# Kernel optimization log

Hardware: AMD Instinct MI355X
Metric: run time of the kernel (lower is better)

Reference implementation:

```python
import jax, jax.numpy as jnp
import numpy as np

N_NODES = 50000
N_EDGES = 819200  # divisible by num_rels=8 -> equal relation segments (implicit rel_ptr)
NUM_RELS = 8
N_HEADS = 4
IN_FEAT = 256
OUT_FEAT = 128
HEAD_DIM = OUT_FEAT // N_HEADS
LEAKY_SLOPE = 0.2


def setup_inputs() -> dict:
    key = jax.random.key(0)
    ks = jax.random.split(key, 7)
    inputs = jax.random.normal(ks[0], (N_NODES, IN_FEAT), dtype=jnp.float32)
    conv_weights = jax.random.normal(ks[1], (NUM_RELS, N_HEADS, IN_FEAT, HEAD_DIM), dtype=jnp.float32) * (1.0 / np.sqrt(IN_FEAT))
    attn_l = jax.random.normal(ks[2], (NUM_RELS, N_HEADS, HEAD_DIM), dtype=jnp.float32) * 0.1
    attn_r = jax.random.normal(ks[3], (NUM_RELS, N_HEADS, HEAD_DIM), dtype=jnp.float32) * 0.1
    h_bias = jax.random.normal(ks[4], (OUT_FEAT,), dtype=jnp.float32) * 0.01
    row_idx = jax.random.randint(ks[5], (N_EDGES,), 0, N_NODES, dtype=jnp.int32)
    col_idx = jax.random.randint(ks[6], (N_EDGES,), 0, N_NODES, dtype=jnp.int32)
    return {
        'inputs': inputs,
        'conv_weights': conv_weights,
        'attn_l': attn_l,
        'attn_r': attn_r,
        'h_bias': h_bias,
        'row_idx': row_idx,
        'col_idx': col_idx,
    }


def reference(inputs, conv_weights, attn_l, attn_r, h_bias, row_idx, col_idx):
    R, H, IN, D = conv_weights.shape
    E = row_idx.shape[0]
    N = inputs.shape[0]
    epr = E // R  # edges per relation (equal segments == rel_ptr)

    # relation-grouped GEMM: per-edge transformed src features [R, epr, H, D]
    src = inputs[row_idx].reshape(R, epr, IN)
    feat_src = jnp.einsum('rei,rhid->rehd', src, conv_weights)
    el = jnp.einsum('rehd,rhd->reh', feat_src, attn_l)

    dst = inputs[col_idx].reshape(R, epr, IN)
    feat_dst = jnp.einsum('rei,rhid->rehd', dst, conv_weights)
    er = jnp.einsum('rehd,rhd->reh', feat_dst, attn_r)

    # fused GAT: leaky_relu(el+er), softmax over incoming edges per dst node
    e = jax.nn.leaky_relu((el + er).reshape(E, H), negative_slope=LEAKY_SLOPE)
    m = jax.ops.segment_max(e, col_idx, num_segments=N)          # [N, H]
    e_exp = jnp.exp(e - m[col_idx])                              # [E, H]
    denom = jax.ops.segment_sum(e_exp, col_idx, num_segments=N)  # [N, H]
    alpha = e_exp / denom[col_idx]                               # [E, H]

    feat = feat_src.reshape(E, H, D)
    h = jax.ops.segment_sum(alpha[:, :, None] * feat, col_idx, num_segments=N)  # [N, H, D]
    h = h.reshape(N, H * D) + h_bias
    # activation=None, self_loop=False, dropout treated as eval (identity)
    return h
```

## Files before the change

### kernel.cpp

```cpp
#include <hip/hip_runtime.h>
#include <hip/hip_bf16.h>

#define N_NODES 50000
#define N_EDGES 819200
#define NUM_RELS 8
#define EPR (N_EDGES / NUM_RELS)
#define N_HEADS 4
#define IN_FEAT 256
#define OUT_FEAT 128
#define HEAD_DIM 32
#define NB_SCAN ((N_NODES + 255) / 256)

typedef __attribute__((ext_vector_type(8))) __bf16 bf16x8;
typedef __attribute__((ext_vector_type(4))) __bf16 bf16x4;
typedef __attribute__((ext_vector_type(4))) float f32x4;

#define SZ_FEAT ((size_t)NUM_RELS * N_NODES * OUT_FEAT)
#define SZ_EL ((size_t)NUM_RELS * N_NODES * N_HEADS)
#define SZ_WB ((size_t)IN_FEAT * 64)
#define SZ_WT ((size_t)NUM_RELS * OUT_FEAT * IN_FEAT / 2)
#define OFF_FEAT ((size_t)0)
#define OFF_XB (OFF_FEAT + SZ_FEAT / 2)
#define OFF_EL (OFF_FEAT + SZ_FEAT)
#define OFF_ER (OFF_EL + SZ_EL)
#define OFF_WB (OFF_ER + SZ_EL)
#define OFF_WT (OFF_WB + SZ_WB)
#define OFF_INT (OFF_WT + SZ_WT)
#define IOFF_CNT ((size_t)0)
#define IOFF_PTR ((size_t)N_NODES)
#define IOFF_CUR ((size_t)2 * N_NODES)
#define IOFF_BSUM ((size_t)3 * N_NODES)
#define IOFF_SPAY ((size_t)3 * N_NODES + 256)

__device__ __forceinline__ void gload16(const void* g, void* l) {
    __builtin_amdgcn_global_load_lds(
        (const __attribute__((address_space(1))) unsigned int*)g,
        (__attribute__((address_space(3))) unsigned int*)l, 16, 0, 0);
}

__global__ void k_cvtx(const float* __restrict__ x, __bf16* __restrict__ xb) {
    int tid = blockIdx.x * blockDim.x + threadIdx.x;
    if (tid >= N_NODES * 32) return;
    int n = tid >> 5, sg = tid & 31;
    const float* xp = x + (size_t)n * IN_FEAT + sg * 8;
    float4 a = *(const float4*)xp;
    float4 b = *(const float4*)(xp + 4);
    bf16x8 v;
    v[0] = (__bf16)a.x; v[1] = (__bf16)a.y; v[2] = (__bf16)a.z; v[3] = (__bf16)a.w;
    v[4] = (__bf16)b.x; v[5] = (__bf16)b.y; v[6] = (__bf16)b.z; v[7] = (__bf16)b.w;
    int slot = (sg & ~7) | ((sg & 7) ^ (n & 7));
    *(bf16x8*)(xb + (size_t)n * 256 + slot * 8) = v;
}

__global__ void k_cvtw(const float* __restrict__ cw, __bf16* __restrict__ wtl) {
    int tid = blockIdx.x * blockDim.x + threadIdx.x;
    if (tid >= 32768) return;
    int s = tid & 3, brow = (tid >> 2) & 127, ks = (tid >> 9) & 1, kc = (tid >> 10) & 3, r = tid >> 12;
    int q = s ^ ((brow >> 1) & 3);
    int k0 = kc * 64 + ks * 32 + q * 8;
    int h = brow >> 5, d = brow & 31;
    const float* src = cw + ((size_t)(r * N_HEADS + h) * IN_FEAT + k0) * HEAD_DIM + d;
    bf16x8 v;
#pragma unroll
    for (int j = 0; j < 8; ++j) v[j] = (__bf16)src[j * HEAD_DIM];
    *(bf16x8*)(wtl + (size_t)tid * 8) = v;
}

__global__ void k_wboth(const float* __restrict__ cw, const float* __restrict__ al,
                        const float* __restrict__ ar, __bf16* __restrict__ wbt) {
    int tid = blockIdx.x * blockDim.x + threadIdx.x;
    if (tid >= IN_FEAT * 64) return;
    int col = tid >> 8, i = tid & 255;
    int side = col >> 5, r = (col >> 2) & 7, h = col & 3;
    const float* av = (side ? ar : al) + (size_t)(r * N_HEADS + h) * HEAD_DIM;
    const float* cwp = cw + ((size_t)(r * N_HEADS + h) * IN_FEAT + i) * HEAD_DIM;
    float s = 0.f;
#pragma unroll
    for (int d = 0; d < HEAD_DIM; ++d) s += cwp[d] * av[d];
    wbt[(size_t)col * IN_FEAT + i] = (__bf16)s;
}

__global__ void k_wbimg(const __bf16* __restrict__ wbt, __bf16* __restrict__ wbl) {
    int tid = blockIdx.x * blockDim.x + threadIdx.x;
    if (tid >= 2048) return;
    int s = tid & 3, brow = (tid >> 2) & 63, ks = (tid >> 8) & 1, kc = tid >> 9;
    int q = s ^ ((brow >> 1) & 3);
    int k0 = kc * 64 + ks * 32 + q * 8;
    bf16x8 v = *(const bf16x8*)(wbt + (size_t)brow * IN_FEAT + k0);
    *(bf16x8*)(wbl + (size_t)tid * 8) = v;
}

__global__ __launch_bounds__(256, 2) void k_fused(const __bf16* __restrict__ xb,
                                                  const __bf16* __restrict__ wtl,
                                                  const __bf16* __restrict__ wbl,
                                                  __bf16* __restrict__ featb,
                                                  float* __restrict__ el,
                                                  float* __restrict__ er) {
    __shared__ __align__(16) unsigned char sA[65536];
    __shared__ __align__(16) unsigned char sB[16384];
    const int t = threadIdx.x, lane = t & 63, w = t >> 6;
    const int wr = w >> 1, wc = w & 1;
    const int n0 = blockIdx.x * 128;

#pragma unroll
    for (int i = 0; i < 16; ++i) {
        int off = i * 4096 + w * 1024 + lane * 16;
        int row = off >> 9;
        int n = n0 + row;
        if (n >= N_NODES) n = N_NODES - 1;
        gload16((const char*)xb + (size_t)n * 512 + (off & 511), sA + i * 4096 + w * 1024);
    }
#pragma unroll
    for (int i = 0; i < 2; ++i)
        gload16((const char*)wtl + i * 4096 + w * 1024 + lane * 16, sB + i * 4096 + w * 1024);

    f32x4 acc[4][4];
#pragma unroll
    for (int i = 0; i < 4; ++i)
#pragma unroll
        for (int j = 0; j < 4; ++j) acc[i][j] = (f32x4){0.f, 0.f, 0.f, 0.f};

    for (int item = 0; item < 64; ++item) {
        const int buf = item & 1;
        if (item < 63) {
            const char* ch = (const char*)wtl + (size_t)(item + 1) * 8192;
#pragma unroll
            for (int i = 0; i < 2; ++i)
                gload16(ch + i * 4096 + w * 1024 + lane * 16, sB + (buf ^ 1) * 8192 + i * 4096 + w * 1024);
            asm volatile("s_waitcnt vmcnt(2)" ::: "memory");
        } else {
            gload16((const char*)wbl + w * 1024 + lane * 16, sB + (buf ^ 1) * 8192 + w * 1024);
            asm volatile("s_waitcnt vmcnt(1)" ::: "memory");
        }
        __builtin_amdgcn_s_barrier();
        __builtin_amdgcn_sched_barrier(0);

        const int r = item >> 3, kc = (item >> 1) & 3, ks = item & 1;
        bf16x8 af[4], bg[4];
#pragma unroll
        for (int rb = 0; rb < 4; ++rb) {
            int row = wr * 64 + rb * 16 + (lane & 15);
            int slot = kc * 8 + ((ks * 4 + (lane >> 4)) ^ (row & 7));
            af[rb] = *(const bf16x8*)(sA + row * 512 + slot * 16);
        }
#pragma unroll
        for (int cb = 0; cb < 4; ++cb) {
            int brow = wc * 64 + cb * 16 + (lane & 15);
            int s = (lane >> 4) ^ ((brow >> 1) & 3);
            bg[cb] = *(const bf16x8*)(sB + buf * 8192 + brow * 64 + s * 16);
        }
#pragma unroll
        for (int rb = 0; rb < 4; ++rb)
#pragma unroll
            for (int cb = 0; cb < 4; ++cb)
                acc[rb][cb] = __builtin_amdgcn_mfma_f32_16x16x32_bf16(af[rb], bg[cb], acc[rb][cb], 0, 0, 0);

        if ((item & 7) == 7) {
#pragma unroll
            for (int rb = 0; rb < 4; ++rb)
#pragma unroll
                for (int q = 0; q < 4; ++q) {
                    int rowi = wr * 64 + rb * 16 + (lane >> 4) * 4 + q;
                    int n = n0 + rowi;
                    if (n < N_NODES) {
                        __bf16* fp = featb + ((size_t)r * N_NODES + n) * OUT_FEAT + wc * 64 + (lane & 15);
#pragma unroll
                        for (int cb = 0; cb < 4; ++cb) fp[cb * 16] = (__bf16)acc[rb][cb][q];
                    }
                }
#pragma unroll
            for (int i = 0; i < 4; ++i)
#pragma unroll
                for (int j = 0; j < 4; ++j) acc[i][j] = (f32x4){0.f, 0.f, 0.f, 0.f};
        }
        asm volatile("" ::: "memory");
        __builtin_amdgcn_s_barrier();
    }

    f32x4 acc2[4][2];
#pragma unroll
    for (int i = 0; i < 4; ++i)
#pragma unroll
        for (int j = 0; j < 2; ++j) acc2[i][j] = (f32x4){0.f, 0.f, 0.f, 0.f};

    for (int e = 0; e < 8; ++e) {
        const int buf = e & 1;
        if (e < 7) {
            gload16((const char*)wbl + (size_t)(e + 1) * 4096 + w * 1024 + lane * 16,
                    sB + (buf ^ 1) * 8192 + w * 1024);
            asm volatile("s_waitcnt vmcnt(1)" ::: "memory");
        } else {
            asm volatile("s_waitcnt vmcnt(0)" ::: "memory");
        }
        __builtin_amdgcn_s_barrier();
        __builtin_amdgcn_sched_barrier(0);

        const int kc = e >> 1, ks = e & 1;
        bf16x8 af[4], bg[2];
#pragma unroll
        for (int rb = 0; rb < 4; ++rb) {
            int row = wr * 64 + rb * 16 + (lane & 15);
            int slot = kc * 8 + ((ks * 4 + (lane >> 4)) ^ (row & 7));
            af[rb] = *(const bf16x8*)(sA + row * 512 + slot * 16);
        }
#pragma unroll
        for (int cb = 0; cb < 2; ++cb) {
            int brow = wc * 32 + cb * 16 + (lane & 15);
            int s = (lane >> 4) ^ ((brow >> 1) & 3);
            bg[cb] = *(const bf16x8*)(sB + buf * 8192 + brow * 64 + s * 16);
        }
#pragma unroll
        for (int rb = 0; rb < 4; ++rb)
#pragma unroll
            for (int cb = 0; cb < 2; ++cb)
                acc2[rb][cb] = __builtin_amdgcn_mfma_f32_16x16x32_bf16(af[rb], bg[cb], acc2[rb][cb], 0, 0, 0);
        asm volatile("" ::: "memory");
        __builtin_amdgcn_s_barrier();
    }
#pragma unroll
    for (int rb = 0; rb < 4; ++rb)
#pragma unroll
        for (int q = 0; q < 4; ++q) {
            int n = n0 + wr * 64 + rb * 16 + (lane >> 4) * 4 + q;
            if (n < N_NODES) {
#pragma unroll
                for (int cb = 0; cb < 2; ++cb) {
                    int c = wc * 32 + cb * 16 + (lane & 15);
                    int side = c >> 5, rr = (c >> 2) & 7, h = c & 3;
                    float* dst = side ? er : el;
                    dst[((size_t)rr * N_NODES + n) * N_HEADS + h] = acc2[rb][cb][q];
                }
            }
        }
}

__global__ void k_hist(const int* __restrict__ col, int* __restrict__ cnt) {
    int e = blockIdx.x * blockDim.x + threadIdx.x;
    if (e < N_EDGES) atomicAdd(cnt + col[e], 1);
}

__global__ __launch_bounds__(256) void k_scanA(const int* __restrict__ cnt,
                                               int* __restrict__ excl,
                                               int* __restrict__ bsum) {
    __shared__ int s[256];
    int i = blockIdx.x * 256 + threadIdx.x;
    int v = (i < N_NODES) ? cnt[i] : 0;
    s[threadIdx.x] = v;
    __syncthreads();
#pragma unroll
    for (int off = 1; off < 256; off <<= 1) {
        int t = (threadIdx.x >= off) ? s[threadIdx.x - off] : 0;
        __syncthreads();
        s[threadIdx.x] += t;
        __syncthreads();
    }
    if (i < N_NODES) excl[i] = s[threadIdx.x] - v;
    if (threadIdx.x == 255) bsum[blockIdx.x] = s[255];
}

__global__ __launch_bounds__(256) void k_scanB(int* __restrict__ bsum) {
    __shared__ int s[256];
    int v = (threadIdx.x < NB_SCAN) ? bsum[threadIdx.x] : 0;
    s[threadIdx.x] = v;
    __syncthreads();
#pragma unroll
    for (int off = 1; off < 256; off <<= 1) {
        int t = (threadIdx.x >= off) ? s[threadIdx.x - off] : 0;
        __syncthreads();
        s[threadIdx.x] += t;
        __syncthreads();
    }
    bsum[threadIdx.x] = s[threadIdx.x] - v;
}

__global__ __launch_bounds__(256) void k_scanC(int* __restrict__ ptr,
                                               int* __restrict__ cursor,
                                               const int* __restrict__ bsum) {
    int i = blockIdx.x * 256 + threadIdx.x;
    if (i >= N_NODES) return;
    int p = ptr[i] + bsum[blockIdx.x];
    ptr[i] = p;
    cursor[i] = p;
}

__global__ void k_scatter(const int* __restrict__ row, const int* __restrict__ col,
                          int* __restrict__ cursor, int* __restrict__ spay) {
    int e = blockIdx.x * blockDim.x + threadIdx.x;
    if (e >= N_EDGES) return;
    int c = col[e];
    int pos = atomicAdd(cursor + c, 1);
    spay[pos] = row[e] | ((e / EPR) << 20);
}

__global__ __launch_bounds__(256) void k_agg(const int* __restrict__ ptr,
                                             const int* __restrict__ cnt,
                                             const int* __restrict__ spay,
                                             const float* __restrict__ el,
                                             const float* __restrict__ er,
                                             const __bf16* __restrict__ featb,
                                             const float* __restrict__ bias,
                                             float* __restrict__ out) {
    const int wv = threadIdx.x >> 6, lane = threadIdx.x & 63;
    const int n = blockIdx.x * 4 + wv;
    if (n >= N_NODES) return;
    const int start = ptr[n], len = cnt[n];
    const int h = lane >> 4;
    float accx = 0.f, accy = 0.f, den = 0.f;
    int j = 0;
    for (; j + 4 <= len; j += 4) {
        int p[4];
#pragma unroll
        for (int u = 0; u < 4; ++u) p[u] = spay[start + j + u];
        float w[4], vx[4], vy[4];
#pragma unroll
        for (int u = 0; u < 4; ++u) {
            int rw = p[u] & 0xFFFFF, r = p[u] >> 20;
            size_t rb = (size_t)r * N_NODES;
            float s = el[(rb + rw) * N_HEADS + h] + er[(rb + n) * N_HEADS + h];
            s = s > 0.f ? s : 0.2f * s;
            w[u] = __expf(s);
            ushort2 raw = *(const ushort2*)(featb + (rb + rw) * OUT_FEAT + lane * 2);
            vx[u] = __uint_as_float((unsigned)raw.x << 16);
            vy[u] = __uint_as_float((unsigned)raw.y << 16);
        }
#pragma unroll
        for (int u = 0; u < 4; ++u) {
            accx += w[u] * vx[u];
            accy += w[u] * vy[u];
            den += w[u];
        }
    }
    for (; j < len; ++j) {
        int p = spay[start + j];
        int rw = p & 0xFFFFF, r = p >> 20;
        size_t rb = (size_t)r * N_NODES;
        float s = el[(rb + rw) * N_HEADS + h] + er[(rb + n) * N_HEADS + h];
        s = s > 0.f ? s : 0.2f * s;
        float w = __expf(s);
        ushort2 raw = *(const ushort2*)(featb + (rb + rw) * OUT_FEAT + lane * 2);
        accx += w * __uint_as_float((unsigned)raw.x << 16);
        accy += w * __uint_as_float((unsigned)raw.y << 16);
        den += w;
    }
    float inv = (len > 0) ? 1.f / den : 0.f;
    int o = lane * 2;
    float2 res;
    res.x = accx * inv + bias[o];
    res.y = accy * inv + bias[o + 1];
    *(float2*)(out + (size_t)n * OUT_FEAT + o) = res;
}

extern "C" void kernel_launch(void* const* d_in, const int* in_sizes, int n_in,
                              void* d_out, int out_size, void* d_ws, size_t ws_size,
                              hipStream_t stream) {
    const float* x = (const float*)d_in[0];
    const float* cw = (const float*)d_in[1];
    const float* al = (const float*)d_in[2];
    const float* ar = (const float*)d_in[3];
    const float* bias = (const float*)d_in[4];
    const int* row = (const int*)d_in[5];
    const int* col = (const int*)d_in[6];
    float* out = (float*)d_out;
    float* ws = (float*)d_ws;

    __bf16* featb = (__bf16*)(ws + OFF_FEAT);
    __bf16* xb = (__bf16*)(ws + OFF_XB);
    float* el = ws + OFF_EL;
    float* er = ws + OFF_ER;
    __bf16* wbt = (__bf16*)(ws + OFF_WB);
    __bf16* wbl = (__bf16*)(ws + OFF_WB + 8192);
    __bf16* wtl = (__bf16*)(ws + OFF_WT);
    int* iw = (int*)(ws + OFF_INT);
    int* cnt = iw + IOFF_CNT;
    int* ptr = iw + IOFF_PTR;
    int* cur = iw + IOFF_CUR;
    int* bsum = iw + IOFF_BSUM;
    int* spay = iw + IOFF_SPAY;

    hipMemsetAsync(cnt, 0, N_NODES * sizeof(int), stream);

    k_cvtx<<<(N_NODES * 32 + 255) / 256, 256, 0, stream>>>(x, xb);
    k_cvtw<<<128, 256, 0, stream>>>(cw, wtl);
    k_wboth<<<(IN_FEAT * 64 + 255) / 256, 256, 0, stream>>>(cw, al, ar, wbt);
    k_wbimg<<<8, 256, 0, stream>>>(wbt, wbl);
    k_fused<<<(N_NODES + 127) / 128, 256, 0, stream>>>(xb, wtl, wbl, featb, el, er);

    k_hist<<<(N_EDGES + 255) / 256, 256, 0, stream>>>(col, cnt);
    k_scanA<<<NB_SCAN, 256, 0, stream>>>(cnt, ptr, bsum);
    k_scanB<<<1, 256, 0, stream>>>(bsum);
    k_scanC<<<NB_SCAN, 256, 0, stream>>>(ptr, cur, bsum);
    k_scatter<<<(N_EDGES + 255) / 256, 256, 0, stream>>>(row, col, cur, spay);

    k_agg<<<(N_NODES + 3) / 4, 256, 0, stream>>>(ptr, cnt, spay, el, er, featb, bias, out);
}
```

Measured before the change: 234.1 us.

## Fuse fp32-to-bf16 input conversion into GEMM kernel and halve node tile

Removes the standalone k_cvtx pass and instead loads fp32 node features directly in k_fused, converting them to bf16 and writing them into the swizzled LDS layout. This avoids writing and re-reading a bf16 copy of the input plus one kernel launch. The node tile shrinks from 128 to 64 rows, so shared memory per block drops and launch bounds now target 3 blocks per CU. The trade-offs are that weight tiles are re-streamed by twice as many blocks and the A-load becomes a synchronous register path instead of async global-to-LDS loads.

```diff
diff --git a/kernel.cpp b/kernel.cpp
--- a/kernel.cpp
+++ b/kernel.cpp
@@ -20,7 +20,6 @@
 #define SZ_WB ((size_t)IN_FEAT * 64)
 #define SZ_WT ((size_t)NUM_RELS * OUT_FEAT * IN_FEAT / 2)
 #define OFF_FEAT ((size_t)0)
-#define OFF_XB (OFF_FEAT + SZ_FEAT / 2)
 #define OFF_EL (OFF_FEAT + SZ_FEAT)
 #define OFF_ER (OFF_EL + SZ_EL)
 #define OFF_WB (OFF_ER + SZ_EL)
@@ -38,20 +37,6 @@
         (__attribute__((address_space(3))) unsigned int*)l, 16, 0, 0);
 }
 
-__global__ void k_cvtx(const float* __restrict__ x, __bf16* __restrict__ xb) {
-    int tid = blockIdx.x * blockDim.x + threadIdx.x;
-    if (tid >= N_NODES * 32) return;
-    int n = tid >> 5, sg = tid & 31;
-    const float* xp = x + (size_t)n * IN_FEAT + sg * 8;
-    float4 a = *(const float4*)xp;
-    float4 b = *(const float4*)(xp + 4);
-    bf16x8 v;
-    v[0] = (__bf16)a.x; v[1] = (__bf16)a.y; v[2] = (__bf16)a.z; v[3] = (__bf16)a.w;
-    v[4] = (__bf16)b.x; v[5] = (__bf16)b.y; v[6] = (__bf16)b.z; v[7] = (__bf16)b.w;
-    int slot = (sg & ~7) | ((sg & 7) ^ (n & 7));
-    *(bf16x8*)(xb + (size_t)n * 256 + slot * 8) = v;
-}
-
 __global__ void k_cvtw(const float* __restrict__ cw, __bf16* __restrict__ wtl) {
     int tid = blockIdx.x * blockDim.x + threadIdx.x;
     if (tid >= 32768) return;
@@ -90,33 +75,41 @@
     *(bf16x8*)(wbl + (size_t)tid * 8) = v;
 }
 
-__global__ __launch_bounds__(256, 2) void k_fused(const __bf16* __restrict__ xb,
+__global__ __launch_bounds__(256, 3) void k_fused(const float* __restrict__ x,
                                                   const __bf16* __restrict__ wtl,
                                                   const __bf16* __restrict__ wbl,
                                                   __bf16* __restrict__ featb,
                                                   float* __restrict__ el,
                                                   float* __restrict__ er) {
-    __shared__ __align__(16) unsigned char sA[65536];
+    __shared__ __align__(16) unsigned char sA[32768];
     __shared__ __align__(16) unsigned char sB[16384];
     const int t = threadIdx.x, lane = t & 63, w = t >> 6;
     const int wr = w >> 1, wc = w & 1;
-    const int n0 = blockIdx.x * 128;
+    const int n0 = blockIdx.x * 64;
+
+#pragma unroll
+    for (int i = 0; i < 2; ++i)
+        gload16((const char*)wtl + i * 4096 + w * 1024 + lane * 16, sB + i * 4096 + w * 1024);
 
 #pragma unroll
     for (int i = 0; i < 16; ++i) {
-        int off = i * 4096 + w * 1024 + lane * 16;
-        int row = off >> 9;
+        int flat = i * 256 + t;
+        int row = flat >> 6;
+        int kq = flat & 63;
         int n = n0 + row;
         if (n >= N_NODES) n = N_NODES - 1;
-        gload16((const char*)xb + (size_t)n * 512 + (off & 511), sA + i * 4096 + w * 1024);
-    }
+        float4 v = *(const float4*)(x + (size_t)n * IN_FEAT + kq * 4);
+        bf16x4 hv;
+        hv[0] = (__bf16)v.x; hv[1] = (__bf16)v.y; hv[2] = (__bf16)v.z; hv[3] = (__bf16)v.w;
+        int sg = kq >> 1;
+        int slot = (sg & ~7) | ((sg & 7) ^ (row & 7));
+        *(bf16x4*)(sA + row * 512 + slot * 16 + (kq & 1) * 8) = hv;
+    }
+    __syncthreads();
+
+    f32x4 acc[2][4];
 #pragma unroll
     for (int i = 0; i < 2; ++i)
-        gload16((const char*)wtl + i * 4096 + w * 1024 + lane * 16, sB + i * 4096 + w * 1024);
-
-    f32x4 acc[4][4];
-#pragma unroll
-    for (int i = 0; i < 4; ++i)
 #pragma unroll
         for (int j = 0; j < 4; ++j) acc[i][j] = (f32x4){0.f, 0.f, 0.f, 0.f};
 
@@ -136,10 +129,10 @@
         __builtin_amdgcn_sched_barrier(0);
 
         const int r = item >> 3, kc = (item >> 1) & 3, ks = item & 1;
-        bf16x8 af[4], bg[4];
-#pragma unroll
-        for (int rb = 0; rb < 4; ++rb) {
-            int row = wr * 64 + rb * 16 + (lane & 15);
+        bf16x8 af[2], bg[4];
+#pragma unroll
+        for (int rb = 0; rb < 2; ++rb) {
+            int row = wr * 32 + rb * 16 + (lane & 15);
             int slot = kc * 8 + ((ks * 4 + (lane >> 4)) ^ (row & 7));
             af[rb] = *(const bf16x8*)(sA + row * 512 + slot * 16);
         }
@@ -150,17 +143,17 @@
             bg[cb] = *(const bf16x8*)(sB + buf * 8192 + brow * 64 + s * 16);
         }
 #pragma unroll
-        for (int rb = 0; rb < 4; ++rb)
+        for (int rb = 0; rb < 2; ++rb)
 #pragma unroll
             for (int cb = 0; cb < 4; ++cb)
                 acc[rb][cb] = __builtin_amdgcn_mfma_f32_16x16x32_bf16(af[rb], bg[cb], acc[rb][cb], 0, 0, 0);
 
         if ((item & 7) == 7) {
 #pragma unroll
-            for (int rb = 0; rb < 4; ++rb)
+            for (int rb = 0; rb < 2; ++rb)
 #pragma unroll
                 for (int q = 0; q < 4; ++q) {
-                    int rowi = wr * 64 + rb * 16 + (lane >> 4) * 4 + q;
+                    int rowi = wr * 32 + rb * 16 + (lane >> 4) * 4 + q;
                     int n = n0 + rowi;
                     if (n < N_NODES) {
                         __bf16* fp = featb + ((size_t)r * N_NODES + n) * OUT_FEAT + wc * 64 + (lane & 15);
@@ -169,7 +162,7 @@
                     }
                 }
 #pragma unroll
-            for (int i = 0; i < 4; ++i)
+            for (int i = 0; i < 2; ++i)
 #pragma unroll
                 for (int j = 0; j < 4; ++j) acc[i][j] = (f32x4){0.f, 0.f, 0.f, 0.f};
         }
@@ -177,9 +170,9 @@
         __builtin_amdgcn_s_barrier();
     }
 
-    f32x4 acc2[4][2];
-#pragma unroll
-    for (int i = 0; i < 4; ++i)
+    f32x4 acc2[2][2];
+#pragma unroll
+    for (int i = 0; i < 2; ++i)
 #pragma unroll
         for (int j = 0; j < 2; ++j) acc2[i][j] = (f32x4){0.f, 0.f, 0.f, 0.f};
 
@@ -196,10 +189,10 @@
         __builtin_amdgcn_sched_barrier(0);
 
         const int kc = e >> 1, ks = e & 1;
-        bf16x8 af[4], bg[2];
-#pragma unroll
-        for (int rb = 0; rb < 4; ++rb) {
-            int row = wr * 64 + rb * 16 + (lane & 15);
+        bf16x8 af[2], bg[2];
+#pragma unroll
+        for (int rb = 0; rb < 2; ++rb) {
+            int row = wr * 32 + rb * 16 + (lane & 15);
             int slot = kc * 8 + ((ks * 4 + (lane >> 4)) ^ (row & 7));
             af[rb] = *(const bf16x8*)(sA + row * 512 + slot * 16);
         }
@@ -210,7 +203,7 @@
             bg[cb] = *(const bf16x8*)(sB + buf * 8192 + brow * 64 + s * 16);
         }
 #pragma unroll
-        for (int rb = 0; rb < 4; ++rb)
+        for (int rb = 0; rb < 2; ++rb)
 #pragma unroll
             for (int cb = 0; cb < 2; ++cb)
                 acc2[rb][cb] = __builtin_amdgcn_mfma_f32_16x16x32_bf16(af[rb], bg[cb], acc2[rb][cb], 0, 0, 0);
@@ -218,10 +211,10 @@
         __builtin_amdgcn_s_barrier();
     }
 #pragma unroll
-    for (int rb = 0; rb < 4; ++rb)
+    for (int rb = 0; rb < 2; ++rb)
 #pragma unroll
         for (int q = 0; q < 4; ++q) {
-            int n = n0 + wr * 64 + rb * 16 + (lane >> 4) * 4 + q;
+            int n = n0 + wr * 32 + rb * 16 + (lane >> 4) * 4 + q;
             if (n < N_NODES) {
 #pragma unroll
                 for (int cb = 0; cb < 2; ++cb) {
@@ -364,7 +357,6 @@
     float* ws = (float*)d_ws;
 
     __bf16* featb = (__bf16*)(ws + OFF_FEAT);
-    __bf16* xb = (__bf16*)(ws + OFF_XB);
     float* el = ws + OFF_EL;
     float* er = ws + OFF_ER;
     __bf16* wbt = (__bf16*)(ws + OFF_WB);
@@ -379,11 +371,10 @@
 
     hipMemsetAsync(cnt, 0, N_NODES * sizeof(int), stream);
 
-    k_cvtx<<<(N_NODES * 32 + 255) / 256, 256, 0, stream>>>(x, xb);
     k_cvtw<<<128, 256, 0, stream>>>(cw, wtl);
     k_wboth<<<(IN_FEAT * 64 + 255) / 256, 256, 0, stream>>>(cw, al, ar, wbt);
     k_wbimg<<<8, 256, 0, stream>>>(wbt, wbl);
-    k_fused<<<(N_NODES + 127) / 128, 256, 0, stream>>>(xb, wtl, wbl, featb, el, er);
+    k_fused<<<(N_NODES + 63) / 64, 256, 0, stream>>>(x, wtl, wbl, featb, el, er);
 
     k_hist<<<(N_EDGES + 255) / 256, 256, 0, stream>>>(col, cnt);
     k_scanA<<<NB_SCAN, 256, 0, stream>>>(cnt, ptr, bsum);
```

Measured after the change: 256.0 us. 1.09x slower.
